# Kernel optimization log

Measured on AMD Instinct MI355X. Metric: run time of the kernel, lower is better.

The kernel has to match this reference:

```python
import jax, jax.numpy as jnp
import numpy as np

B, C, CI, H, W = 8, 256, 128, 48, 48


def conv1x1(x, w, b):
    # x: (B,C,H,W), w: (CI,C), b: (CI,)
    return jnp.einsum('bchw,oc->bohw', x, w) + b[None, :, None, None]


def setup_inputs() -> dict:
    key = jax.random.key(0)
    ks = jax.random.split(key, 14)
    s = 1.0 / np.sqrt(C)
    d = {
        'x_1': jax.random.normal(ks[0], (B, C, H, W), jnp.float32),
        'x_2': jax.random.normal(ks[1], (B, C, H, W), jnp.float32),
    }
    names = ['v1', 'k1', 'q1', 'v2', 'k2', 'q2']
    for i, n in enumerate(names):
        d['w_' + n] = jax.random.uniform(ks[2 + 2 * i], (CI, C), jnp.float32, -s, s)
        d['b_' + n] = jax.random.uniform(ks[3 + 2 * i], (CI,), jnp.float32, -s, s)
    return d


def reference(x_1, x_2, w_v1, b_v1, w_k1, b_k1, w_q1, b_q1,
              w_v2, b_v2, w_k2, b_k2, w_q2, b_q2):
    b, ci, h, w = x_1.shape[0], w_v1.shape[0], x_1.shape[2], x_1.shape[3]
    n = h * w
    V1 = conv1x1(x_1, w_v1, b_v1).reshape(b, ci, n)
    K1 = conv1x1(x_1, w_k1, b_k1).reshape(b, ci, n)
    Q1 = conv1x1(x_1, w_q1, b_q1).reshape(b, ci, n)
    V2 = conv1x1(x_2, w_v2, b_v2).reshape(b, ci, n)
    K2 = conv1x1(x_2, w_k2, b_k2).reshape(b, ci, n)
    Q2 = conv1x1(x_2, w_q2, b_q2).reshape(b, ci, n)
    # sigmoid-gated cross attention, (B, N, N)
    R12 = jax.nn.sigmoid(jnp.einsum('bcn,bcm->bnm', Q1, K2))
    R21 = jax.nn.sigmoid(jnp.einsum('bcn,bcm->bnm', Q2, K1))
    Fu1 = jnp.einsum('bnm,bcm->bcn', R12, V2).reshape(b, ci, h, w)
    Fu2 = jnp.einsum('bnm,bcm->bcn', R21, V1).reshape(b, ci, h, w)
    y_1 = jnp.concatenate([x_1, Fu1], axis=1)
    y_2 = jnp.concatenate([x_2, Fu2], axis=1)
    return (y_1, y_2)
```

## Files before the change

kernel.cpp:

```cpp
#include <hip/hip_runtime.h>
#include <hip/hip_bf16.h>


typedef __bf16 bf16;
typedef __bf16 bf16x8 __attribute__((ext_vector_type(8)));
typedef __bf16 bf16x4 __attribute__((ext_vector_type(4)));
typedef float f32x4 __attribute__((ext_vector_type(4)));
typedef float f32x16 __attribute__((ext_vector_type(16)));

#define NB 8
#define NC 256
#define NCI 128
#define NHW 2304
#define NT32 72

__global__ __launch_bounds__(256) void wconv_kernel(
    const float* __restrict__ w0, const float* __restrict__ w1,
    const float* __restrict__ w2, const float* __restrict__ w3,
    const float* __restrict__ w4, const float* __restrict__ w5,
    bf16* __restrict__ wp)
{
    int g = blockIdx.x * 256 + threadIdx.x;
    int c8 = g & 3;
    int ci = (g >> 2) & 127;
    int stks = g >> 9;
    int st = stks >> 3, ks = stks & 7;
    const float* w = (st == 0) ? w0 : (st == 1) ? w1 : (st == 2) ? w2
                   : (st == 3) ? w3 : (st == 4) ? w4 : w5;
    const float* src = w + ci * NC + ks * 32 + c8 * 8;
    f32x4 a0 = *(const f32x4*)src;
    f32x4 a1 = *(const f32x4*)(src + 4);
    bf16x8 o;
    #pragma unroll
    for (int j = 0; j < 4; ++j) { o[j] = (bf16)a0[j]; o[4 + j] = (bf16)a1[j]; }
    *(bf16x8*)(wp + (size_t)g * 8) = o;
}

__global__ __launch_bounds__(256) void qkv_kernel(
    const float* __restrict__ x1, const float* __restrict__ x2,
    const bf16* __restrict__ wp,
    const float* __restrict__ bv1, const float* __restrict__ bk1, const float* __restrict__ bq1,
    const float* __restrict__ bv2, const float* __restrict__ bk2, const float* __restrict__ bq2,
    bf16* __restrict__ Qp, bf16* __restrict__ Kp, bf16* __restrict__ Vp,
    float* __restrict__ out)
{
    __shared__ __align__(16) bf16 Xt[32 * 264];

    int gid = blockIdx.x;
    int nt = gid % NT32;
    int s = (gid / NT32) & 1;
    int b = gid / (2 * NT32);
    int n0 = nt * 32;

    const float* x = s ? x2 : x1;
    const float* bv = s ? bv2 : bv1;
    const float* bk = s ? bk2 : bk1;
    const float* bq = s ? bq2 : bq1;
    float* outy = out + (size_t)s * (NB * 384 * NHW);

    int tid = threadIdx.x;
    {
        int noff = (tid & 7) * 4;
        int cbase = tid >> 3;
        #pragma unroll
        for (int i = 0; i < 8; ++i) {
            int c = cbase + i * 32;
            const float* src = x + ((size_t)(b * NC + c) * NHW + n0 + noff);
            f32x4 a = *(const f32x4*)src;
            *(f32x4*)(outy + ((size_t)(b * 384 + c) * NHW + n0 + noff)) = a;
            #pragma unroll
            for (int j = 0; j < 4; ++j)
                Xt[(noff + j) * 264 + c] = (bf16)a[j];
        }
    }
    __syncthreads();

    int lane = tid & 63;
    int wid = tid >> 6;
    int row = lane & 15, quad = lane >> 4;

    f32x4 acc[3][2][2];
    #pragma unroll
    for (int t = 0; t < 3; ++t)
        #pragma unroll
        for (int mi = 0; mi < 2; ++mi)
            #pragma unroll
            for (int j = 0; j < 2; ++j)
                acc[t][mi][j] = (f32x4){0.f, 0.f, 0.f, 0.f};

    int stmap[3] = {s * 3 + 2, s * 3 + 1, s * 3 + 0};
    #pragma unroll
    for (int ks = 0; ks < 8; ++ks) {
        bf16x8 bfrag[2];
        int c0 = ks * 32 + quad * 8;
        #pragma unroll
        for (int j = 0; j < 2; ++j)
            bfrag[j] = *(const bf16x8*)&Xt[(j * 16 + row) * 264 + c0];
        #pragma unroll
        for (int t = 0; t < 3; ++t) {
            #pragma unroll
            for (int mi = 0; mi < 2; ++mi) {
                const bf16* wa = wp + (((size_t)(stmap[t] * 8 + ks) * 128 + wid * 32 + mi * 16) * 32)
                               + row * 32 + quad * 8;
                bf16x8 afrag = *(const bf16x8*)wa;
                #pragma unroll
                for (int j = 0; j < 2; ++j)
                    acc[t][mi][j] = __builtin_amdgcn_mfma_f32_16x16x32_bf16(
                        afrag, bfrag[j], acc[t][mi][j], 0, 0, 0);
            }
        }
    }

    size_t qkb = ((size_t)(s * NB + b) * 72 + nt) * 4096;
    int eoff = (quad & 1) * 4;
    int loff = 32 * (quad >> 1);
    #pragma unroll
    for (int mi = 0; mi < 2; ++mi) {
        int ci0 = wid * 32 + mi * 16 + quad * 4;
        int ksl = wid * 2 + mi;
        f32x4 bq4 = *(const f32x4*)&bq[ci0];
        f32x4 bk4 = *(const f32x4*)&bk[ci0];
        f32x4 bv4 = *(const f32x4*)&bv[ci0];
        #pragma unroll
        for (int jj = 0; jj < 2; ++jj) {
            int moff = jj * 16 + row;
            size_t qkoff = qkb + (size_t)ksl * 512 + (size_t)(moff + loff) * 8 + eoff;
            bf16x4 pk;
            #pragma unroll
            for (int r = 0; r < 4; ++r) pk[r] = (bf16)(acc[0][mi][jj][r] + bq4[r]);
            *(bf16x4*)&Qp[qkoff] = pk;
            #pragma unroll
            for (int r = 0; r < 4; ++r) pk[r] = (bf16)(acc[1][mi][jj][r] + bk4[r]);
            *(bf16x4*)&Kp[qkoff] = pk;
            size_t vb = qkb + (size_t)(jj * 4 + wid) * 512
                      + (size_t)(mi * 16 + quad * 4) * 8 + (size_t)(32 * 8) * ((row >> 3) & 1)
                      + (row & 7);
            #pragma unroll
            for (int r = 0; r < 4; ++r)
                Vp[vb + r * 8] = (bf16)(acc[2][mi][jj][r] + bv4[r]);
        }
    }
}

__global__ __launch_bounds__(256, 2) void attn_kernel(
    const bf16* __restrict__ Qp, const bf16* __restrict__ Kp, const bf16* __restrict__ Vp,
    float* __restrict__ out)
{
    __shared__ __align__(16) float CB[8192];

    int gid = blockIdx.x;
    int b = gid & 7;
    int r0 = gid >> 3;
    int dir = r0 & 1;
    int qt = r0 >> 1;
    int n0 = qt * 32;

    int tid = threadIdx.x;
    int lane = tid & 63, w = tid >> 6;
    int l32 = lane & 31, h = lane >> 5;
    bool hb = (h != 0);

    const bf16* qb = Qp + (((size_t)(dir * NB + b) * 72 + qt) * 4096);
    const bf16* kb0 = Kp + ((size_t)((dir ^ 1) * NB + b) * 72) * 4096;
    const bf16* vb0 = Vp + ((size_t)((dir ^ 1) * NB + b) * 72) * 4096;
    float* outy = out + (size_t)dir * (NB * 384 * NHW) + ((size_t)b * 384 + 256) * NHW;

    bf16x8 qf[8];
    #pragma unroll
    for (int ks = 0; ks < 8; ++ks)
        qf[ks] = *(const bf16x8*)&qb[ks * 512 + lane * 8];

    f32x16 o[4];
    #pragma unroll
    for (int ct = 0; ct < 4; ++ct)
        #pragma unroll
        for (int e = 0; e < 16; ++e) o[ct][e] = 0.f;

    union U8 { int i[4]; bf16x8 v; };

    int mb0 = w * 18;
    for (int mb = mb0; mb < mb0 + 18; ++mb) {
        const bf16* kb = kb0 + (size_t)mb * 4096;
        const bf16* vb = vb0 + (size_t)mb * 4096;
        f32x16 sacc;
        #pragma unroll
        for (int e = 0; e < 16; ++e) sacc[e] = 0.f;
        #pragma unroll
        for (int ks = 0; ks < 8; ++ks) {
            bf16x8 kf = *(const bf16x8*)&kb[ks * 512 + lane * 8];
            sacc = __builtin_amdgcn_mfma_f32_32x32x16_bf16(kf, qf[ks], sacc, 0, 0, 0);
        }
        int2 pqi[4];
        #pragma unroll
        for (int g = 0; g < 4; ++g) {
            bf16x4 pq;
            #pragma unroll
            for (int e = 0; e < 4; ++e) {
                float xv = sacc[g * 4 + e];
                float ex = __expf(-xv);
                pq[e] = (bf16)__builtin_amdgcn_rcpf(1.0f + ex);
            }
            pqi[g] = *(int2*)&pq;
        }
        #pragma unroll
        for (int ks2 = 0; ks2 < 2; ++ks2) {
            int2 own  = hb ? pqi[2 * ks2 + 1] : pqi[2 * ks2];
            int2 send = hb ? pqi[2 * ks2]     : pqi[2 * ks2 + 1];
            int2 recv;
            recv.x = __shfl_xor(send.x, 32, 64);
            recv.y = __shfl_xor(send.y, 32, 64);
            int2 lo = hb ? recv : own;
            int2 hi = hb ? own : recv;
            U8 u; u.i[0] = lo.x; u.i[1] = lo.y; u.i[2] = hi.x; u.i[3] = hi.y;
            const bf16* vbs = vb + ks2 * 2048;
            #pragma unroll
            for (int ct = 0; ct < 4; ++ct) {
                bf16x8 vf = *(const bf16x8*)&vbs[ct * 512 + lane * 8];
                o[ct] = __builtin_amdgcn_mfma_f32_32x32x16_bf16(vf, u.v, o[ct], 0, 0, 0);
            }
        }
    }

    __syncthreads();
    if (w >= 2) {
        float* dst = CB + (w - 2) * 4096;
        #pragma unroll
        for (int ct = 0; ct < 4; ++ct)
            #pragma unroll
            for (int g = 0; g < 4; ++g) {
                f32x4 pk;
                #pragma unroll
                for (int e = 0; e < 4; ++e) pk[e] = o[ct][g * 4 + e];
                *(f32x4*)&dst[(ct * 4 + g) * 256 + lane * 4] = pk;
            }
    }
    __syncthreads();
    if (w < 2) {
        const float* src = CB + w * 4096;
        #pragma unroll
        for (int ct = 0; ct < 4; ++ct)
            #pragma unroll
            for (int g = 0; g < 4; ++g) {
                f32x4 pk = *(const f32x4*)&src[(ct * 4 + g) * 256 + lane * 4];
                #pragma unroll
                for (int e = 0; e < 4; ++e) o[ct][g * 4 + e] += pk[e];
            }
    }
    __syncthreads();
    if (w == 0) {
        #pragma unroll
        for (int ct = 2; ct < 4; ++ct)
            #pragma unroll
            for (int g = 0; g < 4; ++g) {
                f32x4 pk;
                #pragma unroll
                for (int e = 0; e < 4; ++e) pk[e] = o[ct][g * 4 + e];
                *(f32x4*)&CB[((ct - 2) * 4 + g) * 256 + lane * 4] = pk;
            }
    } else if (w == 1) {
        #pragma unroll
        for (int ct = 0; ct < 2; ++ct)
            #pragma unroll
            for (int g = 0; g < 4; ++g) {
                f32x4 pk;
                #pragma unroll
                for (int e = 0; e < 4; ++e) pk[e] = o[ct][g * 4 + e];
                *(f32x4*)&CB[2048 + (ct * 4 + g) * 256 + lane * 4] = pk;
            }
    }
    __syncthreads();
    if (w == 0) {
        #pragma unroll
        for (int ct = 0; ct < 2; ++ct)
            #pragma unroll
            for (int g = 0; g < 4; ++g) {
                f32x4 pk = *(const f32x4*)&CB[2048 + (ct * 4 + g) * 256 + lane * 4];
                #pragma unroll
                for (int e = 0; e < 4; ++e) {
                    int c = ct * 32 + e + 8 * g + 4 * h;
                    outy[(size_t)c * NHW + n0 + l32] = pk[e] + o[ct][g * 4 + e];
                }
            }
    } else if (w == 1) {
        #pragma unroll
        for (int ct = 2; ct < 4; ++ct)
            #pragma unroll
            for (int g = 0; g < 4; ++g) {
                f32x4 pk = *(const f32x4*)&CB[((ct - 2) * 4 + g) * 256 + lane * 4];
                #pragma unroll
                for (int e = 0; e < 4; ++e) {
                    int c = ct * 32 + e + 8 * g + 4 * h;
                    outy[(size_t)c * NHW + n0 + l32] = pk[e] + o[ct][g * 4 + e];
                }
            }
    }
}

extern "C" void kernel_launch(void* const* d_in, const int* in_sizes, int n_in,
                              void* d_out, int out_size, void* d_ws, size_t ws_size,
                              hipStream_t stream) {
    const float* x1  = (const float*)d_in[0];
    const float* x2  = (const float*)d_in[1];
    const float* wv1 = (const float*)d_in[2];  const float* bv1 = (const float*)d_in[3];
    const float* wk1 = (const float*)d_in[4];  const float* bk1 = (const float*)d_in[5];
    const float* wq1 = (const float*)d_in[6];  const float* bq1 = (const float*)d_in[7];
    const float* wv2 = (const float*)d_in[8];  const float* bv2 = (const float*)d_in[9];
    const float* wk2 = (const float*)d_in[10]; const float* bk2 = (const float*)d_in[11];
    const float* wq2 = (const float*)d_in[12]; const float* bq2 = (const float*)d_in[13];
    float* out = (float*)d_out;

    size_t per = (size_t)2 * NB * 72 * 4096;
    bf16* Qp = (bf16*)d_ws;
    bf16* Kp = Qp + per;
    bf16* Vp = Kp + per;
    bf16* wp = Vp + per;

    wconv_kernel<<<dim3(96), dim3(256), 0, stream>>>(wv1, wk1, wq1, wv2, wk2, wq2, wp);

    qkv_kernel<<<dim3(NB * 2 * NT32), dim3(256), 0, stream>>>(
        x1, x2, wp, bv1, bk1, bq1, bv2, bk2, bq2, Qp, Kp, Vp, out);

    attn_kernel<<<dim3(NB * 2 * NT32), dim3(256), 0, stream>>>(Qp, Kp, Vp, out);
}
```

Baseline: 282.0 us.

## Process two 32-query tiles per attention block to reuse K/V fragments

Each attention block now handles 64 queries (two 32-row Q tiles) instead of 32, so every K and V fragment loaded from global memory feeds two MFMAs. The grid shrinks from 1152 to 576 blocks and the launch-bound occupancy hint of 2 is removed. This halves K/V load traffic per query but roughly doubles accumulator and Q-fragment register use, which can lower occupancy. It also leaves fewer blocks to spread across the CUs.

```diff
diff --git a/kernel.cpp b/kernel.cpp
--- a/kernel.cpp
+++ b/kernel.cpp
@@ -142,7 +142,7 @@
     }
 }
 
-__global__ __launch_bounds__(256, 2) void attn_kernel(
+__global__ __launch_bounds__(256) void attn_kernel(
     const bf16* __restrict__ Qp, const bf16* __restrict__ Kp, const bf16* __restrict__ Vp,
     float* __restrict__ out)
 {
@@ -152,29 +152,33 @@
     int b = gid & 7;
     int r0 = gid >> 3;
     int dir = r0 & 1;
-    int qt = r0 >> 1;
-    int n0 = qt * 32;
+    int q64 = r0 >> 1;
+    int n0 = q64 * 64;
 
     int tid = threadIdx.x;
     int lane = tid & 63, w = tid >> 6;
     int l32 = lane & 31, h = lane >> 5;
     bool hb = (h != 0);
 
-    const bf16* qb = Qp + (((size_t)(dir * NB + b) * 72 + qt) * 4096);
+    const bf16* qb  = Qp + (((size_t)(dir * NB + b) * 72 + q64 * 2) * 4096);
     const bf16* kb0 = Kp + ((size_t)((dir ^ 1) * NB + b) * 72) * 4096;
     const bf16* vb0 = Vp + ((size_t)((dir ^ 1) * NB + b) * 72) * 4096;
     float* outy = out + (size_t)dir * (NB * 384 * NHW) + ((size_t)b * 384 + 256) * NHW;
 
-    bf16x8 qf[8];
-    #pragma unroll
-    for (int ks = 0; ks < 8; ++ks)
-        qf[ks] = *(const bf16x8*)&qb[ks * 512 + lane * 8];
-
-    f32x16 o[4];
-    #pragma unroll
-    for (int ct = 0; ct < 4; ++ct)
-        #pragma unroll
-        for (int e = 0; e < 16; ++e) o[ct][e] = 0.f;
+    bf16x8 qf[2][8];
+    #pragma unroll
+    for (int t = 0; t < 2; ++t)
+        #pragma unroll
+        for (int ks = 0; ks < 8; ++ks)
+            qf[t][ks] = *(const bf16x8*)&qb[t * 4096 + ks * 512 + lane * 8];
+
+    f32x16 o[2][4];
+    #pragma unroll
+    for (int t = 0; t < 2; ++t)
+        #pragma unroll
+        for (int ct = 0; ct < 4; ++ct)
+            #pragma unroll
+            for (int e = 0; e < 16; ++e) o[t][ct][e] = 0.f;
 
     union U8 { int i[4]; bf16x8 v; };
 
@@ -182,117 +186,131 @@
     for (int mb = mb0; mb < mb0 + 18; ++mb) {
         const bf16* kb = kb0 + (size_t)mb * 4096;
         const bf16* vb = vb0 + (size_t)mb * 4096;
-        f32x16 sacc;
-        #pragma unroll
-        for (int e = 0; e < 16; ++e) sacc[e] = 0.f;
+        f32x16 sacc[2];
+        #pragma unroll
+        for (int t = 0; t < 2; ++t)
+            #pragma unroll
+            for (int e = 0; e < 16; ++e) sacc[t][e] = 0.f;
         #pragma unroll
         for (int ks = 0; ks < 8; ++ks) {
             bf16x8 kf = *(const bf16x8*)&kb[ks * 512 + lane * 8];
-            sacc = __builtin_amdgcn_mfma_f32_32x32x16_bf16(kf, qf[ks], sacc, 0, 0, 0);
-        }
-        int2 pqi[4];
-        #pragma unroll
-        for (int g = 0; g < 4; ++g) {
-            bf16x4 pq;
-            #pragma unroll
-            for (int e = 0; e < 4; ++e) {
-                float xv = sacc[g * 4 + e];
-                float ex = __expf(-xv);
-                pq[e] = (bf16)__builtin_amdgcn_rcpf(1.0f + ex);
+            sacc[0] = __builtin_amdgcn_mfma_f32_32x32x16_bf16(kf, qf[0][ks], sacc[0], 0, 0, 0);
+            sacc[1] = __builtin_amdgcn_mfma_f32_32x32x16_bf16(kf, qf[1][ks], sacc[1], 0, 0, 0);
+        }
+        int2 pqi[2][4];
+        #pragma unroll
+        for (int t = 0; t < 2; ++t) {
+            #pragma unroll
+            for (int g = 0; g < 4; ++g) {
+                bf16x4 pq;
+                #pragma unroll
+                for (int e = 0; e < 4; ++e) {
+                    float xv = sacc[t][g * 4 + e];
+                    float ex = __expf(-xv);
+                    pq[e] = (bf16)__builtin_amdgcn_rcpf(1.0f + ex);
+                }
+                pqi[t][g] = *(int2*)&pq;
             }
-            pqi[g] = *(int2*)&pq;
         }
         #pragma unroll
         for (int ks2 = 0; ks2 < 2; ++ks2) {
-            int2 own  = hb ? pqi[2 * ks2 + 1] : pqi[2 * ks2];
-            int2 send = hb ? pqi[2 * ks2]     : pqi[2 * ks2 + 1];
-            int2 recv;
-            recv.x = __shfl_xor(send.x, 32, 64);
-            recv.y = __shfl_xor(send.y, 32, 64);
-            int2 lo = hb ? recv : own;
-            int2 hi = hb ? own : recv;
-            U8 u; u.i[0] = lo.x; u.i[1] = lo.y; u.i[2] = hi.x; u.i[3] = hi.y;
+            U8 u[2];
+            #pragma unroll
+            for (int t = 0; t < 2; ++t) {
+                int2 own  = hb ? pqi[t][2 * ks2 + 1] : pqi[t][2 * ks2];
+                int2 send = hb ? pqi[t][2 * ks2]     : pqi[t][2 * ks2 + 1];
+                int2 recv;
+                recv.x = __shfl_xor(send.x, 32, 64);
+                recv.y = __shfl_xor(send.y, 32, 64);
+                int2 lo = hb ? recv : own;
+                int2 hi = hb ? own : recv;
+                u[t].i[0] = lo.x; u[t].i[1] = lo.y; u[t].i[2] = hi.x; u[t].i[3] = hi.y;
+            }
             const bf16* vbs = vb + ks2 * 2048;
             #pragma unroll
             for (int ct = 0; ct < 4; ++ct) {
                 bf16x8 vf = *(const bf16x8*)&vbs[ct * 512 + lane * 8];
-                o[ct] = __builtin_amdgcn_mfma_f32_32x32x16_bf16(vf, u.v, o[ct], 0, 0, 0);
+                o[0][ct] = __builtin_amdgcn_mfma_f32_32x32x16_bf16(vf, u[0].v, o[0][ct], 0, 0, 0);
+                o[1][ct] = __builtin_amdgcn_mfma_f32_32x32x16_bf16(vf, u[1].v, o[1][ct], 0, 0, 0);
             }
         }
     }
 
-    __syncthreads();
-    if (w >= 2) {
-        float* dst = CB + (w - 2) * 4096;
-        #pragma unroll
-        for (int ct = 0; ct < 4; ++ct)
-            #pragma unroll
-            for (int g = 0; g < 4; ++g) {
-                f32x4 pk;
-                #pragma unroll
-                for (int e = 0; e < 4; ++e) pk[e] = o[ct][g * 4 + e];
-                *(f32x4*)&dst[(ct * 4 + g) * 256 + lane * 4] = pk;
-            }
-    }
-    __syncthreads();
-    if (w < 2) {
-        const float* src = CB + w * 4096;
-        #pragma unroll
-        for (int ct = 0; ct < 4; ++ct)
-            #pragma unroll
-            for (int g = 0; g < 4; ++g) {
-                f32x4 pk = *(const f32x4*)&src[(ct * 4 + g) * 256 + lane * 4];
-                #pragma unroll
-                for (int e = 0; e < 4; ++e) o[ct][g * 4 + e] += pk[e];
-            }
-    }
-    __syncthreads();
-    if (w == 0) {
-        #pragma unroll
-        for (int ct = 2; ct < 4; ++ct)
-            #pragma unroll
-            for (int g = 0; g < 4; ++g) {
-                f32x4 pk;
-                #pragma unroll
-                for (int e = 0; e < 4; ++e) pk[e] = o[ct][g * 4 + e];
-                *(f32x4*)&CB[((ct - 2) * 4 + g) * 256 + lane * 4] = pk;
-            }
-    } else if (w == 1) {
-        #pragma unroll
-        for (int ct = 0; ct < 2; ++ct)
-            #pragma unroll
-            for (int g = 0; g < 4; ++g) {
-                f32x4 pk;
-                #pragma unroll
-                for (int e = 0; e < 4; ++e) pk[e] = o[ct][g * 4 + e];
-                *(f32x4*)&CB[2048 + (ct * 4 + g) * 256 + lane * 4] = pk;
-            }
-    }
-    __syncthreads();
-    if (w == 0) {
-        #pragma unroll
-        for (int ct = 0; ct < 2; ++ct)
-            #pragma unroll
-            for (int g = 0; g < 4; ++g) {
-                f32x4 pk = *(const f32x4*)&CB[2048 + (ct * 4 + g) * 256 + lane * 4];
-                #pragma unroll
-                for (int e = 0; e < 4; ++e) {
-                    int c = ct * 32 + e + 8 * g + 4 * h;
-                    outy[(size_t)c * NHW + n0 + l32] = pk[e] + o[ct][g * 4 + e];
-                }
-            }
-    } else if (w == 1) {
-        #pragma unroll
-        for (int ct = 2; ct < 4; ++ct)
-            #pragma unroll
-            for (int g = 0; g < 4; ++g) {
-                f32x4 pk = *(const f32x4*)&CB[((ct - 2) * 4 + g) * 256 + lane * 4];
-                #pragma unroll
-                for (int e = 0; e < 4; ++e) {
-                    int c = ct * 32 + e + 8 * g + 4 * h;
-                    outy[(size_t)c * NHW + n0 + l32] = pk[e] + o[ct][g * 4 + e];
-                }
-            }
+    for (int t = 0; t < 2; ++t) {
+        int nq = n0 + t * 32;
+        __syncthreads();
+        if (w >= 2) {
+            float* dst = CB + (w - 2) * 4096;
+            #pragma unroll
+            for (int ct = 0; ct < 4; ++ct)
+                #pragma unroll
+                for (int g = 0; g < 4; ++g) {
+                    f32x4 pk;
+                    #pragma unroll
+                    for (int e = 0; e < 4; ++e) pk[e] = o[t][ct][g * 4 + e];
+                    *(f32x4*)&dst[(ct * 4 + g) * 256 + lane * 4] = pk;
+                }
+        }
+        __syncthreads();
+        if (w < 2) {
+            const float* src = CB + w * 4096;
+            #pragma unroll
+            for (int ct = 0; ct < 4; ++ct)
+                #pragma unroll
+                for (int g = 0; g < 4; ++g) {
+                    f32x4 pk = *(const f32x4*)&src[(ct * 4 + g) * 256 + lane * 4];
+                    #pragma unroll
+                    for (int e = 0; e < 4; ++e) o[t][ct][g * 4 + e] += pk[e];
+                }
+        }
+        __syncthreads();
+        if (w == 0) {
+            #pragma unroll
+            for (int ct = 2; ct < 4; ++ct)
+                #pragma unroll
+                for (int g = 0; g < 4; ++g) {
+                    f32x4 pk;
+                    #pragma unroll
+                    for (int e = 0; e < 4; ++e) pk[e] = o[t][ct][g * 4 + e];
+                    *(f32x4*)&CB[((ct - 2) * 4 + g) * 256 + lane * 4] = pk;
+                }
+        } else if (w == 1) {
+            #pragma unroll
+            for (int ct = 0; ct < 2; ++ct)
+                #pragma unroll
+                for (int g = 0; g < 4; ++g) {
+                    f32x4 pk;
+                    #pragma unroll
+                    for (int e = 0; e < 4; ++e) pk[e] = o[t][ct][g * 4 + e];
+                    *(f32x4*)&CB[2048 + (ct * 4 + g) * 256 + lane * 4] = pk;
+                }
+        }
+        __syncthreads();
+        if (w == 0) {
+            #pragma unroll
+            for (int ct = 0; ct < 2; ++ct)
+                #pragma unroll
+                for (int g = 0; g < 4; ++g) {
+                    f32x4 pk = *(const f32x4*)&CB[2048 + (ct * 4 + g) * 256 + lane * 4];
+                    #pragma unroll
+                    for (int e = 0; e < 4; ++e) {
+                        int c = ct * 32 + e + 8 * g + 4 * h;
+                        outy[(size_t)c * NHW + nq + l32] = pk[e] + o[t][ct][g * 4 + e];
+                    }
+                }
+        } else if (w == 1) {
+            #pragma unroll
+            for (int ct = 2; ct < 4; ++ct)
+                #pragma unroll
+                for (int g = 0; g < 4; ++g) {
+                    f32x4 pk = *(const f32x4*)&CB[((ct - 2) * 4 + g) * 256 + lane * 4];
+                    #pragma unroll
+                    for (int e = 0; e < 4; ++e) {
+                        int c = ct * 32 + e + 8 * g + 4 * h;
+                        outy[(size_t)c * NHW + nq + l32] = pk[e] + o[t][ct][g * 4 + e];
+                    }
+                }
+        }
     }
 }
 
@@ -320,5 +338,5 @@
     qkv_kernel<<<dim3(NB * 2 * NT32), dim3(256), 0, stream>>>(
         x1, x2, wp, bv1, bk1, bq1, bv2, bk2, bq2, Qp, Kp, Vp, out);
 
-    attn_kernel<<<dim3(NB * 2 * NT32), dim3(256), 0, stream>>>(Qp, Kp, Vp, out);
+    attn_kernel<<<dim3(NB * 2 * 36), dim3(256), 0, stream>>>(Qp, Kp, Vp, out);
 }
```

Result: slower. 333.0 us (+18.1%).
